# Kernel optimization log

Measured on AMD Instinct MI355X. Metric: run time of the kernel, lower is better.

Reference implementation:

```python
import jax, jax.numpy as jnp
import numpy as np

N = 100000      # nodes
DEG = 16        # in-degree per node
E = N * DEG     # edges
D = 64          # feature dim (indim == outdim)
L2_EPS = 1e-12  # F.normalize eps


def setup_inputs() -> dict:
    key = jax.random.key(0)
    k1, k2, k3, k4 = jax.random.split(key, 4)
    h = jax.random.normal(k1, (N, D), dtype=jnp.float32)
    e = jax.random.normal(k2, (E, D), dtype=jnp.float32)
    norm = jax.random.uniform(k3, (N, 1), dtype=jnp.float32, minval=0.1, maxval=1.0)
    src = jax.random.randint(k4, (E,), 0, N, dtype=jnp.int32)
    # every node receives exactly DEG incoming edges (sorted dst)
    dst = jnp.repeat(jnp.arange(N, dtype=jnp.int32), DEG)
    return {"h": h, "e": e, "norm": norm, "src": src, "dst": dst}


def reference(h, e, norm, src, dst):
    n = h.shape[0]
    # dropout(p=0) is identity; h = h * norm; Ah = Bh = h
    hn = h * norm                                    # [N, D]
    # message: e_ij = Ce + Bh_src + Bh_dst ; Ah_j = Ah_src
    e_ij = e + hn[src] + hn[dst]                     # [E, D]
    msg = jax.nn.relu(jax.nn.sigmoid(e_ij) * hn[src])  # gated + activation
    # reduce: per-destination max over incoming messages
    c = jax.ops.segment_max(msg, dst, num_segments=n)  # [N, D]
    # update (apply_node_func): no 'b' yet -> bundle = cat(h, c)
    bundle = jnp.concatenate([hn, c], axis=1)        # [N, 2D]
    l2 = jnp.linalg.norm(bundle, axis=1, keepdims=True)
    bundle = bundle / jnp.maximum(l2, L2_EPS)        # F.normalize(p=2, dim=1)
    b = jax.nn.relu(bundle)
    # h <- c, then h = h * norm ; e <- activation(e_ij) ; batch_norm=False
    h_out = c * norm
    e_out = jax.nn.relu(e_ij)
    return (h_out, b, e_out)
```

## Files before the change

### kernel.cpp

```cpp
#include <hip/hip_runtime.h>
#include <cfloat>
#include <cmath>


typedef float f4 __attribute__((ext_vector_type(4)));

__device__ __forceinline__ f4 f4max(f4 a, f4 b) {
    f4 r;
    r.x = fmaxf(a.x, b.x); r.y = fmaxf(a.y, b.y);
    r.z = fmaxf(a.z, b.z); r.w = fmaxf(a.w, b.w);
    return r;
}
__device__ __forceinline__ f4 f4relu(f4 a) {
    f4 r;
    r.x = fmaxf(a.x, 0.f); r.y = fmaxf(a.y, 0.f);
    r.z = fmaxf(a.z, 0.f); r.w = fmaxf(a.w, 0.f);
    return r;
}
__device__ __forceinline__ float sigmoidf_(float x) {
    return 1.0f / (1.0f + __expf(-x));
}
__device__ __forceinline__ f4 f4sig(f4 x) {
    f4 r;
    r.x = sigmoidf_(x.x); r.y = sigmoidf_(x.y);
    r.z = sigmoidf_(x.z); r.w = sigmoidf_(x.w);
    return r;
}
__device__ __forceinline__ f4 shfl_xor_f4(f4 v, int m) {
    v.x = __shfl_xor(v.x, m); v.y = __shfl_xor(v.y, m);
    v.z = __shfl_xor(v.z, m); v.w = __shfl_xor(v.w, m);
    return v;
}

__global__ __launch_bounds__(256, 8) void gnn_fused(
    const float* __restrict__ h,
    const float* __restrict__ e,
    const float* __restrict__ norm,
    const int*   __restrict__ src,
    float*       __restrict__ out,
    int n)
{
    const int wid = (blockIdx.x * 256 + threadIdx.x) >> 6;
    if (wid >= n) return;
    const int lane = threadIdx.x & 63;
    const int q = lane & 15;
    const int g = lane >> 4;

    const long ebase = (long)wid * 16;
    const f4* __restrict__ h4 = (const f4*)h;

    const int   sv   = src[ebase + q];
    const float nrm  = norm[wid];
    const f4    hraw = h4[(size_t)wid * 16 + q];

    const f4* __restrict__ e4 = (const f4*)e + ebase * 16;
    const f4 ev0 = __builtin_nontemporal_load(e4 + 0 * 64 + lane);
    const f4 ev1 = __builtin_nontemporal_load(e4 + 1 * 64 + lane);
    const f4 ev2 = __builtin_nontemporal_load(e4 + 2 * 64 + lane);
    const f4 ev3 = __builtin_nontemporal_load(e4 + 3 * 64 + lane);

    const f4 hni = hraw * nrm;

    f4* __restrict__ eo4 = (f4*)(out + (size_t)n * 192) + ebase * 16;
    f4 cmax = {-FLT_MAX, -FLT_MAX, -FLT_MAX, -FLT_MAX};

#define EDGE(T, EV)                                                         \
    {                                                                       \
        const int s = __shfl(sv, (T) * 4 + g);                              \
        const float ns = norm[s];                                           \
        const f4 hs = h4[(size_t)s * 16 + q] * ns;        \
        const f4 eij = (EV) + hs + hni;                                     \
        __builtin_nontemporal_store(f4relu(eij), eo4 + (T) * 64 + lane);    \
        cmax = f4max(cmax, f4relu(f4sig(eij) * hs));                        \
    }

    EDGE(0, ev0)
    EDGE(1, ev1)
    EDGE(2, ev2)
    EDGE(3, ev3)
#undef EDGE

    cmax = f4max(cmax, shfl_xor_f4(cmax, 16));
    cmax = f4max(cmax, shfl_xor_f4(cmax, 32));

    float ss = hni.x * hni.x + hni.y * hni.y + hni.z * hni.z + hni.w * hni.w
             + cmax.x * cmax.x + cmax.y * cmax.y + cmax.z * cmax.z + cmax.w * cmax.w;
    ss += __shfl_xor(ss, 1);
    ss += __shfl_xor(ss, 2);
    ss += __shfl_xor(ss, 4);
    ss += __shfl_xor(ss, 8);
    const float scale = 1.0f / fmaxf(sqrtf(ss), 1e-12f);

    f4* __restrict__ b4 = (f4*)(out + (size_t)n * 64);
    if (g == 0) {
        __builtin_nontemporal_store(cmax * nrm, (f4*)out + (size_t)wid * 16 + q);
        __builtin_nontemporal_store(f4relu(hni * scale), b4 + (size_t)wid * 32 + q);
    } else if (g == 1) {
        __builtin_nontemporal_store(f4relu(cmax * scale), b4 + (size_t)wid * 32 + 16 + q);
    }
}

extern "C" void kernel_launch(void* const* d_in, const int* in_sizes, int n_in,
                              void* d_out, int out_size, void* d_ws, size_t ws_size,
                              hipStream_t stream) {
    const float* h    = (const float*)d_in[0];
    const float* e    = (const float*)d_in[1];
    const float* norm = (const float*)d_in[2];
    const int*   src  = (const int*)d_in[3];
    float* out = (float*)d_out;

    const int n = in_sizes[0] / 64;
    const int blocks = (n * 64 + 255) / 256;

    gnn_fused<<<blocks, 256, 0, stream>>>(h, e, norm, src, out, n);
}
```

Before: 187.1 us.

## Precompute normalized node features in bf16 and process two nodes per wavefront

Adds a prepass kernel that computes h*norm once per node and stores it as bf16 in workspace, so the main kernel gathers half-size rows and no longer does a per-edge norm lookup. The main kernel now handles two destination nodes per wavefront, issuing eight edge loads and all gathers up front to raise memory-level parallelism, with occupancy hint lowered. The cost is an extra launch and a round trip through workspace. bf16 rounding of hn also changes output precision, which may exceed tolerance. The pairing reads past the end when n is odd.

New measurement: 175.1 us. -6.4%, faster.

```diff
diff --git a/kernel.cpp b/kernel.cpp
--- a/kernel.cpp
+++ b/kernel.cpp
@@ -4,6 +4,9 @@
 
 
 typedef float f4 __attribute__((ext_vector_type(4)));
+typedef float f8 __attribute__((ext_vector_type(8)));
+typedef unsigned short u16x4 __attribute__((ext_vector_type(4)));
+typedef unsigned short u16x8 __attribute__((ext_vector_type(8)));
 
 __device__ __forceinline__ f4 f4max(f4 a, f4 b) {
     f4 r;
@@ -31,72 +34,143 @@
     v.z = __shfl_xor(v.z, m); v.w = __shfl_xor(v.w, m);
     return v;
 }
+__device__ __forceinline__ unsigned short bf16_rne(float f) {
+    unsigned u = __float_as_uint(f);
+    u += 0x7FFFu + ((u >> 16) & 1u);
+    return (unsigned short)(u >> 16);
+}
+__device__ __forceinline__ f4 bf4_dec(u16x4 u) {
+    f4 r;
+    r.x = __uint_as_float((unsigned)u.x << 16);
+    r.y = __uint_as_float((unsigned)u.y << 16);
+    r.z = __uint_as_float((unsigned)u.z << 16);
+    r.w = __uint_as_float((unsigned)u.w << 16);
+    return r;
+}
 
-__global__ __launch_bounds__(256, 8) void gnn_fused(
+__global__ __launch_bounds__(256) void hn_prepass(
     const float* __restrict__ h,
+    const float* __restrict__ norm,
+    u16x8* __restrict__ hnb,
+    int n8)
+{
+    const int i = blockIdx.x * 256 + threadIdx.x;
+    if (i >= n8) return;
+    const f8 v = __builtin_nontemporal_load((const f8*)h + i);
+    const float nr = norm[i >> 3];
+    u16x8 o;
+    o.s0 = bf16_rne(v.s0 * nr); o.s1 = bf16_rne(v.s1 * nr);
+    o.s2 = bf16_rne(v.s2 * nr); o.s3 = bf16_rne(v.s3 * nr);
+    o.s4 = bf16_rne(v.s4 * nr); o.s5 = bf16_rne(v.s5 * nr);
+    o.s6 = bf16_rne(v.s6 * nr); o.s7 = bf16_rne(v.s7 * nr);
+    hnb[i] = o;
+}
+
+__global__ __launch_bounds__(256, 4) void gnn_main2(
     const float* __restrict__ e,
     const float* __restrict__ norm,
     const int*   __restrict__ src,
+    const u16x4* __restrict__ hnb,
     float*       __restrict__ out,
     int n)
 {
-    const int wid = (blockIdx.x * 256 + threadIdx.x) >> 6;
-    if (wid >= n) return;
+    const int wp = (blockIdx.x * 256 + threadIdx.x) >> 6;
+    const int npairs = (n + 1) >> 1;
+    if (wp >= npairs) return;
     const int lane = threadIdx.x & 63;
     const int q = lane & 15;
     const int g = lane >> 4;
 
-    const long ebase = (long)wid * 16;
-    const f4* __restrict__ h4 = (const f4*)h;
+    const int node0 = 2 * wp;
+    const int node1 = 2 * wp + 1;
+    const long ebase = (long)wp * 32;
 
-    const int   sv   = src[ebase + q];
-    const float nrm  = norm[wid];
-    const f4    hraw = h4[(size_t)wid * 16 + q];
+    const int   src32 = __builtin_nontemporal_load(src + ebase + (lane & 31));
+    const float nrm0  = norm[node0];
+    const float nrm1  = norm[node1];
+    const u16x4 hbi0  = hnb[(size_t)node0 * 16 + q];
+    const u16x4 hbi1  = hnb[(size_t)node1 * 16 + q];
 
     const f4* __restrict__ e4 = (const f4*)e + ebase * 16;
     const f4 ev0 = __builtin_nontemporal_load(e4 + 0 * 64 + lane);
     const f4 ev1 = __builtin_nontemporal_load(e4 + 1 * 64 + lane);
     const f4 ev2 = __builtin_nontemporal_load(e4 + 2 * 64 + lane);
     const f4 ev3 = __builtin_nontemporal_load(e4 + 3 * 64 + lane);
+    const f4 ev4 = __builtin_nontemporal_load(e4 + 4 * 64 + lane);
+    const f4 ev5 = __builtin_nontemporal_load(e4 + 5 * 64 + lane);
+    const f4 ev6 = __builtin_nontemporal_load(e4 + 6 * 64 + lane);
+    const f4 ev7 = __builtin_nontemporal_load(e4 + 7 * 64 + lane);
 
-    const f4 hni = hraw * nrm;
+    const int sa0 = __shfl(src32,  0 + g);
+    const int sa1 = __shfl(src32,  4 + g);
+    const int sa2 = __shfl(src32,  8 + g);
+    const int sa3 = __shfl(src32, 12 + g);
+    const int sb0 = __shfl(src32, 16 +  0 + g);
+    const int sb1 = __shfl(src32, 16 +  4 + g);
+    const int sb2 = __shfl(src32, 16 +  8 + g);
+    const int sb3 = __shfl(src32, 16 + 12 + g);
+
+    const u16x4 ha0 = hnb[(size_t)sa0 * 16 + q];
+    const u16x4 ha1 = hnb[(size_t)sa1 * 16 + q];
+    const u16x4 ha2 = hnb[(size_t)sa2 * 16 + q];
+    const u16x4 ha3 = hnb[(size_t)sa3 * 16 + q];
+    const u16x4 hb0 = hnb[(size_t)sb0 * 16 + q];
+    const u16x4 hb1 = hnb[(size_t)sb1 * 16 + q];
+    const u16x4 hb2 = hnb[(size_t)sb2 * 16 + q];
+    const u16x4 hb3 = hnb[(size_t)sb3 * 16 + q];
+
+    const f4 hni0 = bf4_dec(hbi0);
+    const f4 hni1 = bf4_dec(hbi1);
 
     f4* __restrict__ eo4 = (f4*)(out + (size_t)n * 192) + ebase * 16;
-    f4 cmax = {-FLT_MAX, -FLT_MAX, -FLT_MAX, -FLT_MAX};
+    f4 cmax0 = {-FLT_MAX, -FLT_MAX, -FLT_MAX, -FLT_MAX};
+    f4 cmax1 = cmax0;
 
-#define EDGE(T, EV)                                                         \
-    {                                                                       \
-        const int s = __shfl(sv, (T) * 4 + g);                              \
-        const float ns = norm[s];                                           \
-        const f4 hs = h4[(size_t)s * 16 + q] * ns;        \
-        const f4 eij = (EV) + hs + hni;                                     \
-        __builtin_nontemporal_store(f4relu(eij), eo4 + (T) * 64 + lane);    \
-        cmax = f4max(cmax, f4relu(f4sig(eij) * hs));                        \
+#define EDGE(T, EV, HB, HNI, CM)                                             \
+    {                                                                        \
+        const f4 hs = bf4_dec(HB);                                           \
+        const f4 eij = (EV) + hs + (HNI);                                    \
+        __builtin_nontemporal_store(f4relu(eij), eo4 + (T) * 64 + lane);     \
+        CM = f4max(CM, f4relu(f4sig(eij) * hs));                             \
     }
 
-    EDGE(0, ev0)
-    EDGE(1, ev1)
-    EDGE(2, ev2)
-    EDGE(3, ev3)
+    EDGE(0, ev0, ha0, hni0, cmax0)
+    EDGE(4, ev4, hb0, hni1, cmax1)
+    EDGE(1, ev1, ha1, hni0, cmax0)
+    EDGE(5, ev5, hb1, hni1, cmax1)
+    EDGE(2, ev2, ha2, hni0, cmax0)
+    EDGE(6, ev6, hb2, hni1, cmax1)
+    EDGE(3, ev3, ha3, hni0, cmax0)
+    EDGE(7, ev7, hb3, hni1, cmax1)
 #undef EDGE
 
-    cmax = f4max(cmax, shfl_xor_f4(cmax, 16));
-    cmax = f4max(cmax, shfl_xor_f4(cmax, 32));
+    cmax0 = f4max(cmax0, shfl_xor_f4(cmax0, 16));
+    cmax0 = f4max(cmax0, shfl_xor_f4(cmax0, 32));
+    cmax1 = f4max(cmax1, shfl_xor_f4(cmax1, 16));
+    cmax1 = f4max(cmax1, shfl_xor_f4(cmax1, 32));
 
-    float ss = hni.x * hni.x + hni.y * hni.y + hni.z * hni.z + hni.w * hni.w
-             + cmax.x * cmax.x + cmax.y * cmax.y + cmax.z * cmax.z + cmax.w * cmax.w;
-    ss += __shfl_xor(ss, 1);
-    ss += __shfl_xor(ss, 2);
-    ss += __shfl_xor(ss, 4);
-    ss += __shfl_xor(ss, 8);
-    const float scale = 1.0f / fmaxf(sqrtf(ss), 1e-12f);
+    float ss0 = hni0.x * hni0.x + hni0.y * hni0.y + hni0.z * hni0.z + hni0.w * hni0.w
+              + cmax0.x * cmax0.x + cmax0.y * cmax0.y + cmax0.z * cmax0.z + cmax0.w * cmax0.w;
+    float ss1 = hni1.x * hni1.x + hni1.y * hni1.y + hni1.z * hni1.z + hni1.w * hni1.w
+              + cmax1.x * cmax1.x + cmax1.y * cmax1.y + cmax1.z * cmax1.z + cmax1.w * cmax1.w;
+    ss0 += __shfl_xor(ss0, 1); ss1 += __shfl_xor(ss1, 1);
+    ss0 += __shfl_xor(ss0, 2); ss1 += __shfl_xor(ss1, 2);
+    ss0 += __shfl_xor(ss0, 4); ss1 += __shfl_xor(ss1, 4);
+    ss0 += __shfl_xor(ss0, 8); ss1 += __shfl_xor(ss1, 8);
+    const float scale0 = 1.0f / fmaxf(sqrtf(ss0), 1e-12f);
+    const float scale1 = 1.0f / fmaxf(sqrtf(ss1), 1e-12f);
 
+    f4 bv;
+    if (g == 0)      bv = f4relu(hni0 * scale0);
+    else if (g == 1) bv = f4relu(cmax0 * scale0);
+    else if (g == 2) bv = f4relu(hni1 * scale1);
+    else             bv = f4relu(cmax1 * scale1);
     f4* __restrict__ b4 = (f4*)(out + (size_t)n * 64);
-    if (g == 0) {
-        __builtin_nontemporal_store(cmax * nrm, (f4*)out + (size_t)wid * 16 + q);
-        __builtin_nontemporal_store(f4relu(hni * scale), b4 + (size_t)wid * 32 + q);
-    } else if (g == 1) {
-        __builtin_nontemporal_store(f4relu(cmax * scale), b4 + (size_t)wid * 32 + 16 + q);
+    __builtin_nontemporal_store(bv, b4 + (size_t)node0 * 32 + lane);
+
+    if (g < 2) {
+        const f4 hv = (g == 0) ? (cmax0 * nrm0) : (cmax1 * nrm1);
+        __builtin_nontemporal_store(hv, (f4*)out + (size_t)node0 * 16 + lane);
     }
 }
 
@@ -110,7 +184,11 @@
     float* out = (float*)d_out;
 
     const int n = in_sizes[0] / 64;
-    const int blocks = (n * 64 + 255) / 256;
+    const int npairs = (n + 1) >> 1;
+    const int blocks = (npairs * 64 + 255) / 256;
 
-    gnn_fused<<<blocks, 256, 0, stream>>>(h, e, norm, src, out, n);
+    u16x8* hnb8 = (u16x8*)d_ws;
+    const int n8 = n * 8;
+    hn_prepass<<<(n8 + 255) / 256, 256, 0, stream>>>(h, norm, hnb8, n8);
+    gnn_main2<<<blocks, 256, 0, stream>>>(e, norm, src, (const u16x4*)d_ws, out, n);
 }
```
